# Kernel optimization log

Hardware: AMD Instinct MI355X
Metric: run time of the kernel (lower is better)

Reference implementation:

```python
import jax, jax.numpy as jnp
import numpy as np

B, T, D, H = 2, 2048, 1024, 16
DH = D // H  # 64, rope dim


def rotate_half(x):
    x1, x2 = jnp.split(x, 2, axis=-1)
    return jnp.concatenate([-x2, x1], axis=-1)


def rope_tables(seq_len, dim, dtype=jnp.float32):
    inv_freq = 1.0 / (10000.0 ** (jnp.arange(0, dim, 2, dtype=jnp.float32) / dim))
    t = jnp.arange(seq_len, dtype=jnp.float32)
    freqs = jnp.outer(t, inv_freq)              # [T, dim/2]
    emb = jnp.concatenate([freqs, freqs], -1)   # [T, dim]
    return jnp.cos(emb).astype(dtype), jnp.sin(emb).astype(dtype)


def setup_inputs() -> dict:
    key = jax.random.key(0)
    ks = jax.random.split(key, 5)
    w_scale = 0.02
    x = jax.random.normal(ks[0], (B, T, D), jnp.float32)
    W_q = jax.random.normal(ks[1], (D, D), jnp.float32) * w_scale
    W_k = jax.random.normal(ks[2], (D, D), jnp.float32) * w_scale
    W_v = jax.random.normal(ks[3], (D, D), jnp.float32) * w_scale
    W_o = jax.random.normal(ks[4], (D, D), jnp.float32) * w_scale
    mask = jnp.tril(jnp.ones((T, T), jnp.int32))  # causal
    return {"x": x, "W_q": W_q, "W_k": W_k, "W_v": W_v, "W_o": W_o, "mask": mask}


def reference(x, W_q, W_k, W_v, W_o, mask):
    b, t, d = x.shape
    # Linear (bias=False): y = x @ W^T, weight shape (out, in)
    def proj(W):
        y = jnp.einsum('btd,ed->bte', x, W)
        return y.reshape(b, t, H, DH).transpose(0, 2, 1, 3)  # [B,H,T,dh]
    q, k, v = proj(W_q), proj(W_k), proj(W_v)

    cos, sin = rope_tables(t, DH, x.dtype)
    cos = cos[None, None]  # [1,1,T,dh]
    sin = sin[None, None]
    q = q * cos + rotate_half(q) * sin
    k = k * cos + rotate_half(k) * sin

    scale = 1.0 / np.sqrt(DH).astype(np.float32)
    scores = jnp.einsum('bhqd,bhkd->bhqk', q, k) * scale  # [B,H,T,T]
    neg_inf = jnp.finfo(scores.dtype).min
    scores = jnp.where(mask[:t, :t][None, None] == 0, neg_inf, scores)
    attn = jax.nn.softmax(scores, axis=-1)
    out = jnp.einsum('bhqk,bhkd->bhqd', attn, v)
    out = out.transpose(0, 2, 1, 3).reshape(b, t, d)
    return jnp.einsum('btd,ed->bte', out, W_o)
```

## Files before the change

kernel.cpp:

```cpp
#include <hip/hip_runtime.h>
#include <hip/hip_bf16.h>
#include <math.h>

#define B_  2
#define T_  2048
#define D_  1024
#define H_  16
#define DH_ 64
#define WN_ (D_ * D_)

typedef __attribute__((ext_vector_type(8))) short bf16x8;
typedef __attribute__((ext_vector_type(4))) float f32x4;
typedef __attribute__((ext_vector_type(16))) float f32x16;

__device__ __forceinline__ void gll16(const void* g, void* l) {
  __builtin_amdgcn_global_load_lds(
      (const __attribute__((address_space(1))) void*)g,
      (__attribute__((address_space(3))) void*)l, 16, 0, 0);
}

__device__ __forceinline__ void storeC(float* p, float v) { *p = v; }
__device__ __forceinline__ void storeC(__hip_bfloat16* p, float v) {
  *p = __float2bfloat16(v);
}

__global__ __launch_bounds__(256)
void cvt_f32_bf16(const float* __restrict__ in, __hip_bfloat16* __restrict__ out,
                  int n4) {
  const int i = blockIdx.x * 256 + threadIdx.x;
  if (i >= n4) return;
  const float4 a = ((const float4*)in)[i];
  __hip_bfloat16 h0 = __float2bfloat16(a.x);
  __hip_bfloat16 h1 = __float2bfloat16(a.y);
  __hip_bfloat16 h2 = __float2bfloat16(a.z);
  __hip_bfloat16 h3 = __float2bfloat16(a.w);
  ushort4 o;
  o.x = *(unsigned short*)&h0;
  o.y = *(unsigned short*)&h1;
  o.z = *(unsigned short*)&h2;
  o.w = *(unsigned short*)&h3;
  *(ushort4*)(out + (size_t)i * 4) = o;
}

__global__ __launch_bounds__(256)
void cvt3_w(const float* __restrict__ Wq, const float* __restrict__ Wk,
            const float* __restrict__ Wv, __hip_bfloat16* __restrict__ out) {
  const int i = blockIdx.x * 256 + threadIdx.x;
  const int per = WN_ / 4;
  const int sel = i >> 18;
  const int off = i & (per - 1);
  const float* src = sel == 0 ? Wq : (sel == 1 ? Wk : Wv);
  const float4 a = ((const float4*)src)[off];
  __hip_bfloat16 h0 = __float2bfloat16(a.x);
  __hip_bfloat16 h1 = __float2bfloat16(a.y);
  __hip_bfloat16 h2 = __float2bfloat16(a.z);
  __hip_bfloat16 h3 = __float2bfloat16(a.w);
  ushort4 o;
  o.x = *(unsigned short*)&h0;
  o.y = *(unsigned short*)&h1;
  o.z = *(unsigned short*)&h2;
  o.w = *(unsigned short*)&h3;
  *(ushort4*)(out + (size_t)sel * WN_ + (size_t)off * 4) = o;
}

template <typename CT>
__global__ __launch_bounds__(256)
void gemm_bf16_mfma(const __hip_bfloat16* __restrict__ A,
                    const __hip_bfloat16* __restrict__ W,
                    CT* __restrict__ C, int M, int N, int K) {
  __shared__ unsigned short As[128 * 32];
  __shared__ unsigned short Bs[128 * 32];
  const int tid = threadIdx.x;
  const int w = tid >> 6;
  const int lane = tid & 63;
  const int lg = lane >> 4;
  const int ln = lane & 15;
  const int wr = w >> 1, wc = w & 1;
  const int row0 = blockIdx.y * 128;
  const int col0 = blockIdx.x * 128;

  const int sr = w * 32 + (lane >> 2);
  const int sp = lane & 3;

  f32x4 acc[4][4];
#pragma unroll
  for (int m = 0; m < 4; ++m)
#pragma unroll
    for (int n = 0; n < 4; ++n) acc[m][n] = (f32x4){0.f, 0.f, 0.f, 0.f};

  for (int k0 = 0; k0 < K; k0 += 32) {
#pragma unroll
    for (int c = 0; c < 2; ++c) {
      const int r = sr + c * 16;
      const int ks = sp ^ ((r >> 1) & 3);
      gll16(A + (size_t)(row0 + r) * K + k0 + ks * 8,
            &As[(w * 32 + c * 16) * 32]);
      gll16(W + (size_t)(col0 + r) * K + k0 + ks * 8,
            &Bs[(w * 32 + c * 16) * 32]);
    }
    __syncthreads();

    bf16x8 af[4], bfr[4];
#pragma unroll
    for (int m = 0; m < 4; ++m) {
      const int r = wr * 64 + m * 16 + ln;
      af[m] = *(const bf16x8*)&As[r * 32 + (lg ^ ((r >> 1) & 3)) * 8];
    }
#pragma unroll
    for (int n = 0; n < 4; ++n) {
      const int r = wc * 64 + n * 16 + ln;
      bfr[n] = *(const bf16x8*)&Bs[r * 32 + (lg ^ ((r >> 1) & 3)) * 8];
    }
#pragma unroll
    for (int m = 0; m < 4; ++m)
#pragma unroll
      for (int n = 0; n < 4; ++n)
        acc[m][n] = __builtin_amdgcn_mfma_f32_16x16x32_bf16(af[m], bfr[n],
                                                            acc[m][n], 0, 0, 0);
    __syncthreads();
  }

#pragma unroll
  for (int m = 0; m < 4; ++m) {
#pragma unroll
    for (int reg = 0; reg < 4; ++reg) {
      CT* crow = C + (size_t)(row0 + wr * 64 + m * 16 + lg * 4 + reg) * N
                 + col0 + wc * 64;
#pragma unroll
      for (int n = 0; n < 4; ++n) storeC(&crow[n * 16 + ln], acc[m][n][reg]);
    }
  }
}

__global__ __launch_bounds__(256)
void rope_qkv(const __hip_bfloat16* __restrict__ qkv,
              __hip_bfloat16* __restrict__ Qb, __hip_bfloat16* __restrict__ Kb) {
  const int idx = blockIdx.x * 256 + threadIdx.x;
  const int i = idx & 31;
  const int rest = idx >> 5;
  const int row = rest >> 4;
  const int h = rest & 15;
  const int t = row & (T_ - 1);
  const float inv_freq = powf(10000.0f, -(float)i * (1.0f / 32.0f));
  const float ang = (float)t * inv_freq;
  const float c = cosf(ang), s = sinf(ang);
  const size_t rb = (size_t)row * 3072 + h * 64;
  const float q1 = __bfloat162float(qkv[rb + i]);
  const float q2 = __bfloat162float(qkv[rb + i + 32]);
  const float k1 = __bfloat162float(qkv[rb + 1024 + i]);
  const float k2 = __bfloat162float(qkv[rb + 1024 + i + 32]);
  const size_t base = (size_t)rest * DH_;
  Qb[base + i]      = __float2bfloat16((q1 * c - q2 * s) * 0.125f);
  Qb[base + i + 32] = __float2bfloat16((q2 * c + q1 * s) * 0.125f);
  Kb[base + i]      = __float2bfloat16(k1 * c - k2 * s);
  Kb[base + i + 32] = __float2bfloat16(k2 * c + k1 * s);
}

__global__ __launch_bounds__(256)
void kf_prep(const __hip_bfloat16* __restrict__ kb, __hip_bfloat16* __restrict__ Kf) {
  const int kt = blockIdx.x;
  const int bh = blockIdx.y;
  const int b = bh >> 4, h = bh & 15;
  const int tid = threadIdx.x;
  const int j = tid & 7;
  const int t0 = tid >> 3;
  __hip_bfloat16* dsth = Kf + (size_t)bh * (T_ * 64) + (size_t)kt * 4096;
#pragma unroll
  for (int it = 0; it < 2; ++it) {
    const int t = it * 32 + t0;
    bf16x8 x = *(const bf16x8*)(kb +
        (size_t)(((size_t)b * T_ + kt * 64 + t) * H_ + h) * 64 + j * 8);
    const int kb2 = t >> 5, lane31 = t & 31, ks = j >> 1, hi = j & 1;
    *(bf16x8*)(dsth + (((kb2 * 4 + ks) * 64 + hi * 32 + lane31) * 8)) = x;
  }
}

__global__ __launch_bounds__(256)
void vf_prep(const __hip_bfloat16* __restrict__ qkv, __hip_bfloat16* __restrict__ Vf) {
  __shared__ unsigned short Ls[64][72];
  const int kt = blockIdx.x;
  const int bh = blockIdx.y;
  const int b = bh >> 4, h = bh & 15;
  const int tid = threadIdx.x;
  const int rb = tid >> 3, c0 = (tid & 7) * 8;
#pragma unroll
  for (int it = 0; it < 2; ++it) {
    const int r = it * 32 + rb;
    uint4 x = *(const uint4*)&qkv[(size_t)((size_t)b * T_ + kt * 64 + r) * 3072 +
                                  2048 + h * 64 + c0];
    const unsigned short* xs = (const unsigned short*)&x;
#pragma unroll
    for (int q = 0; q < 8; ++q) Ls[c0 + q][r] = xs[q];
  }
  __syncthreads();
  __hip_bfloat16* dsth = Vf + (size_t)bh * (T_ * 64) + (size_t)kt * 4096;
#pragma unroll
  for (int e = 0; e < 2; ++e) {
    const int g = e * 256 + tid;
    const int lane31 = g & 31, hi = (g >> 5) & 1, ks = (g >> 6) & 3, kb2 = g >> 8;
    bf16x8 x = *(const bf16x8*)&Ls[kb2 * 32 + lane31][ks * 16 + hi * 8];
    *(bf16x8*)(dsth + (size_t)g * 8) = x;
  }
}

#define SWZ(row, col) ((col) ^ (((row) & 7) << 3))

struct KV { bf16x8 k[2][4]; bf16x8 v[2][4]; };

__global__ __launch_bounds__(256, 2)
void attn_reg(const __hip_bfloat16* __restrict__ Qb,
              const __hip_bfloat16* __restrict__ Kf,
              const __hip_bfloat16* __restrict__ Vf,
              __hip_bfloat16* __restrict__ O) {
  __shared__ unsigned short Ps[4][32 * 64];

  const int bx = blockIdx.x;
  const int bh = blockIdx.y;
  const int b = bh >> 4, h = bh & 15;
  const int tid = threadIdx.x;
  const int w = tid >> 6;
  const int lane = tid & 63;
  const int lq = lane & 31;
  const int hi = lane >> 5;

  const int qu = (w < 2) ? (2 * bx + w) : (62 - 2 * bx + (w & 1));
  const int nt = (qu >> 1) + 1;
  const int q_glob = qu * 32 + lq;

  const size_t headoff = (size_t)b * T_ * D_ + (size_t)h * DH_;
  const __hip_bfloat16* Qg = Qb + headoff;
  const __hip_bfloat16* Kfh = Kf + (size_t)bh * (T_ * 64);
  const __hip_bfloat16* Vfh = Vf + (size_t)bh * (T_ * 64);
  __hip_bfloat16* Og = O + headoff;

  bf16x8 qf[4];
#pragma unroll
  for (int ks = 0; ks < 4; ++ks)
    qf[ks] = *(const bf16x8*)(Qg + (size_t)q_glob * D_ + ks * 16 + hi * 8);

  float m_run = -3.0e38f, l_run = 0.f;
  f32x16 accO[2];
#pragma unroll
  for (int reg = 0; reg < 16; ++reg) { accO[0][reg] = 0.f; accO[1][reg] = 0.f; }

  auto load = [&](int kt) {
    KV r;
    const __hip_bfloat16* kp = Kfh + (size_t)kt * 4096;
    const __hip_bfloat16* vp = Vfh + (size_t)kt * 4096;
#pragma unroll
    for (int kb2 = 0; kb2 < 2; ++kb2)
#pragma unroll
      for (int ks = 0; ks < 4; ++ks) {
        r.k[kb2][ks] = *(const bf16x8*)(kp + ((kb2 * 4 + ks) * 64 + lane) * 8);
        r.v[kb2][ks] = *(const bf16x8*)(vp + ((kb2 * 4 + ks) * 64 + lane) * 8);
      }
    return r;
  };

  auto compute = [&](const KV& kv, int kt) {
    f32x16 sf[2];
#pragma unroll
    for (int reg = 0; reg < 16; ++reg) { sf[0][reg] = 0.f; sf[1][reg] = 0.f; }
    const bool last = (kt == nt - 1);
    const bool skip1 = last && !(qu & 1);
#pragma unroll
    for (int ks = 0; ks < 4; ++ks)
      sf[0] = __builtin_amdgcn_mfma_f32_32x32x16_bf16(kv.k[0][ks], qf[ks], sf[0], 0, 0, 0);
    if (!skip1) {
#pragma unroll
      for (int ks = 0; ks < 4; ++ks)
        sf[1] = __builtin_amdgcn_mfma_f32_32x32x16_bf16(kv.k[1][ks], qf[ks], sf[1], 0, 0, 0);
    }

    if (last) {
      const int kv0 = kt * 64;
#pragma unroll
      for (int reg = 0; reg < 16; ++reg) {
        const int krow = (reg & 3) + 8 * (reg >> 2) + 4 * hi;
        if (kv0 + krow > q_glob)      sf[0][reg] = -3.0e38f;
        if (kv0 + 32 + krow > q_glob) sf[1][reg] = -3.0e38f;
      }
    }

    float pmax = -3.0e38f;
#pragma unroll
    for (int reg = 0; reg < 16; ++reg)
      pmax = fmaxf(pmax, fmaxf(sf[0][reg], sf[1][reg]));
    pmax = fmaxf(pmax, __shfl_xor(pmax, 32, 64));
    const float mnew = fmaxf(m_run, pmax);
    const float alpha = __expf(m_run - mnew);
    m_run = mnew;
    float rsum = 0.f;
#pragma unroll
    for (int reg = 0; reg < 16; ++reg) {
      sf[0][reg] = __expf(sf[0][reg] - mnew);
      sf[1][reg] = __expf(sf[1][reg] - mnew);
      rsum += sf[0][reg] + sf[1][reg];
    }
    rsum += __shfl_xor(rsum, 32, 64);
    l_run = l_run * alpha + rsum;
#pragma unroll
    for (int reg = 0; reg < 16; ++reg) {
      accO[0][reg] *= alpha;
      accO[1][reg] *= alpha;
    }

#pragma unroll
    for (int kb2 = 0; kb2 < 2; ++kb2) {
#pragma unroll
      for (int j = 0; j < 4; ++j) {
        __hip_bfloat16 b0 = __float2bfloat16(sf[kb2][4 * j + 0]);
        __hip_bfloat16 b1 = __float2bfloat16(sf[kb2][4 * j + 1]);
        __hip_bfloat16 b2 = __float2bfloat16(sf[kb2][4 * j + 2]);
        __hip_bfloat16 b3 = __float2bfloat16(sf[kb2][4 * j + 3]);
        uint2 pk;
        pk.x = (unsigned)*(unsigned short*)&b0 |
               ((unsigned)*(unsigned short*)&b1 << 16);
        pk.y = (unsigned)*(unsigned short*)&b2 |
               ((unsigned)*(unsigned short*)&b3 << 16);
        const int col = kb2 * 32 + 8 * j + 4 * hi;
        *(uint2*)&Ps[w][lq * 64 + SWZ(lq, col)] = pk;
      }
    }

#pragma unroll
    for (int ks = 0; ks < 4; ++ks) {
      const int c = ks * 16 + hi * 8;
      bf16x8 pb = *(const bf16x8*)&Ps[w][lq * 64 + SWZ(lq, c)];
      accO[0] = __builtin_amdgcn_mfma_f32_32x32x16_bf16(kv.v[0][ks], pb, accO[0], 0, 0, 0);
      accO[1] = __builtin_amdgcn_mfma_f32_32x32x16_bf16(kv.v[1][ks], pb, accO[1], 0, 0, 0);
    }
  };

  KV bufA = load(0), bufB;
  int kt = 0;
  while (true) {
    if (kt + 1 < nt) bufB = load(kt + 1);
    compute(bufA, kt);
    ++kt; if (kt == nt) break;
    if (kt + 1 < nt) bufA = load(kt + 1);
    compute(bufB, kt);
    ++kt; if (kt == nt) break;
  }

  const float inv = 1.0f / l_run;
#pragma unroll
  for (int db = 0; db < 2; ++db) {
#pragma unroll
    for (int j = 0; j < 4; ++j) {
      __hip_bfloat16 b0 = __float2bfloat16(accO[db][4 * j + 0] * inv);
      __hip_bfloat16 b1 = __float2bfloat16(accO[db][4 * j + 1] * inv);
      __hip_bfloat16 b2 = __float2bfloat16(accO[db][4 * j + 2] * inv);
      __hip_bfloat16 b3 = __float2bfloat16(accO[db][4 * j + 3] * inv);
      uint2 pk;
      pk.x = (unsigned)*(unsigned short*)&b0 |
             ((unsigned)*(unsigned short*)&b1 << 16);
      pk.y = (unsigned)*(unsigned short*)&b2 |
             ((unsigned)*(unsigned short*)&b3 << 16);
      const int d = db * 32 + 8 * j + 4 * hi;
      *(uint2*)(Og + (size_t)q_glob * D_ + d) = pk;
    }
  }
}

extern "C" void kernel_launch(void* const* d_in, const int* in_sizes, int n_in,
                              void* d_out, int out_size, void* d_ws, size_t ws_size,
                              hipStream_t stream) {
  const float* x  = (const float*)d_in[0];
  const float* Wq = (const float*)d_in[1];
  const float* Wk = (const float*)d_in[2];
  const float* Wv = (const float*)d_in[3];
  const float* Wo = (const float*)d_in[4];
  float* out = (float*)d_out;

  const size_t NE = (size_t)B_ * T_ * D_;
  char* base = (char*)d_ws;
  __hip_bfloat16* qkvb  = (__hip_bfloat16*)base;
  __hip_bfloat16* xb    = (__hip_bfloat16*)(base + 3 * NE * 2);
  __hip_bfloat16* Wqkvb = (__hip_bfloat16*)(base + 4 * NE * 2);
  __hip_bfloat16* qb    = (__hip_bfloat16*)(base + 4 * NE * 2 + 3ull * WN_ * 2);
  __hip_bfloat16* kb    = qb + NE;
  __hip_bfloat16* Kfb   = kb + NE;
  __hip_bfloat16* Vfb   = Kfb + NE;
  __hip_bfloat16* aob   = qkvb;
  __hip_bfloat16* Wob   = Wqkvb;

  cvt_f32_bf16<<<(int)(NE / 4 / 256), 256, 0, stream>>>(x, xb, (int)(NE / 4));
  cvt3_w<<<3 * WN_ / 4 / 256, 256, 0, stream>>>(Wq, Wk, Wv, Wqkvb);

  const dim3 gq(3 * D_ / 128, (B_ * T_) / 128);
  gemm_bf16_mfma<__hip_bfloat16><<<gq, 256, 0, stream>>>(
      xb, Wqkvb, qkvb, B_ * T_, 3 * D_, D_);

  rope_qkv<<<(B_ * T_ * H_ * 32) / 256, 256, 0, stream>>>(qkvb, qb, kb);
  kf_prep<<<dim3(T_ / 64, B_ * H_), 256, 0, stream>>>(kb, Kfb);
  vf_prep<<<dim3(T_ / 64, B_ * H_), 256, 0, stream>>>(qkvb, Vfb);

  const dim3 ga(16, B_ * H_);
  attn_reg<<<ga, 256, 0, stream>>>(qb, Kfb, Vfb, aob);

  cvt_f32_bf16<<<WN_ / 4 / 256, 256, 0, stream>>>(Wo, Wob, WN_ / 4);

  const dim3 go(D_ / 128, (B_ * T_) / 128);
  gemm_bf16_mfma<float><<<go, 256, 0, stream>>>(aob, Wob, out, B_ * T_, D_, D_);
}
```

Baseline: 234.0 us.

## Split attention KV range across wave pairs and fuse RoPE with K layout prep

The attention kernel now gives each block two query tiles and splits each tile's causal KV range between two waves. The partial accumulators, max and sum are merged through shared memory, and the launch doubles to 1024 blocks with a swizzled block order and occupancy hint 3. RoPE now uses vectorized 8-wide loads and writes K directly in the MFMA-friendly layout, which removes the separate kf_prep kernel and its intermediate buffer. This is meant to raise parallelism and balance the causal work, at the cost of extra LDS for the merge and a block-wide sync.

```diff
diff --git a/kernel.cpp b/kernel.cpp
--- a/kernel.cpp
+++ b/kernel.cpp
@@ -24,21 +24,27 @@
   *p = __float2bfloat16(v);
 }
 
+__device__ __forceinline__ float bf2f(short u) {
+  union { unsigned int i; float f; } cv;
+  cv.i = ((unsigned int)(unsigned short)u) << 16;
+  return cv.f;
+}
+__device__ __forceinline__ short f2bf(float f) {
+  __hip_bfloat16 h = __float2bfloat16(f);
+  return *(short*)&h;
+}
+
 __global__ __launch_bounds__(256)
 void cvt_f32_bf16(const float* __restrict__ in, __hip_bfloat16* __restrict__ out,
                   int n4) {
   const int i = blockIdx.x * 256 + threadIdx.x;
   if (i >= n4) return;
   const float4 a = ((const float4*)in)[i];
-  __hip_bfloat16 h0 = __float2bfloat16(a.x);
-  __hip_bfloat16 h1 = __float2bfloat16(a.y);
-  __hip_bfloat16 h2 = __float2bfloat16(a.z);
-  __hip_bfloat16 h3 = __float2bfloat16(a.w);
   ushort4 o;
-  o.x = *(unsigned short*)&h0;
-  o.y = *(unsigned short*)&h1;
-  o.z = *(unsigned short*)&h2;
-  o.w = *(unsigned short*)&h3;
+  o.x = (unsigned short)f2bf(a.x);
+  o.y = (unsigned short)f2bf(a.y);
+  o.z = (unsigned short)f2bf(a.z);
+  o.w = (unsigned short)f2bf(a.w);
   *(ushort4*)(out + (size_t)i * 4) = o;
 }
 
@@ -51,15 +57,11 @@
   const int off = i & (per - 1);
   const float* src = sel == 0 ? Wq : (sel == 1 ? Wk : Wv);
   const float4 a = ((const float4*)src)[off];
-  __hip_bfloat16 h0 = __float2bfloat16(a.x);
-  __hip_bfloat16 h1 = __float2bfloat16(a.y);
-  __hip_bfloat16 h2 = __float2bfloat16(a.z);
-  __hip_bfloat16 h3 = __float2bfloat16(a.w);
   ushort4 o;
-  o.x = *(unsigned short*)&h0;
-  o.y = *(unsigned short*)&h1;
-  o.z = *(unsigned short*)&h2;
-  o.w = *(unsigned short*)&h3;
+  o.x = (unsigned short)f2bf(a.x);
+  o.y = (unsigned short)f2bf(a.y);
+  o.z = (unsigned short)f2bf(a.z);
+  o.w = (unsigned short)f2bf(a.w);
   *(ushort4*)(out + (size_t)sel * WN_ + (size_t)off * 4) = o;
 }
 
@@ -133,46 +135,45 @@
 }
 
 __global__ __launch_bounds__(256)
-void rope_qkv(const __hip_bfloat16* __restrict__ qkv,
-              __hip_bfloat16* __restrict__ Qb, __hip_bfloat16* __restrict__ Kb) {
+void rope_fused(const __hip_bfloat16* __restrict__ qkv,
+                __hip_bfloat16* __restrict__ Qb,
+                __hip_bfloat16* __restrict__ Kf) {
   const int idx = blockIdx.x * 256 + threadIdx.x;
-  const int i = idx & 31;
-  const int rest = idx >> 5;
+  const int j = idx & 3;
+  const int rest = idx >> 2;
+  const int h = rest & 15;
   const int row = rest >> 4;
-  const int h = rest & 15;
   const int t = row & (T_ - 1);
-  const float inv_freq = powf(10000.0f, -(float)i * (1.0f / 32.0f));
-  const float ang = (float)t * inv_freq;
-  const float c = cosf(ang), s = sinf(ang);
-  const size_t rb = (size_t)row * 3072 + h * 64;
-  const float q1 = __bfloat162float(qkv[rb + i]);
-  const float q2 = __bfloat162float(qkv[rb + i + 32]);
-  const float k1 = __bfloat162float(qkv[rb + 1024 + i]);
-  const float k2 = __bfloat162float(qkv[rb + 1024 + i + 32]);
-  const size_t base = (size_t)rest * DH_;
-  Qb[base + i]      = __float2bfloat16((q1 * c - q2 * s) * 0.125f);
-  Qb[base + i + 32] = __float2bfloat16((q2 * c + q1 * s) * 0.125f);
-  Kb[base + i]      = __float2bfloat16(k1 * c - k2 * s);
-  Kb[base + i + 32] = __float2bfloat16(k2 * c + k1 * s);
-}
-
-__global__ __launch_bounds__(256)
-void kf_prep(const __hip_bfloat16* __restrict__ kb, __hip_bfloat16* __restrict__ Kf) {
-  const int kt = blockIdx.x;
-  const int bh = blockIdx.y;
-  const int b = bh >> 4, h = bh & 15;
-  const int tid = threadIdx.x;
-  const int j = tid & 7;
-  const int t0 = tid >> 3;
-  __hip_bfloat16* dsth = Kf + (size_t)bh * (T_ * 64) + (size_t)kt * 4096;
-#pragma unroll
-  for (int it = 0; it < 2; ++it) {
-    const int t = it * 32 + t0;
-    bf16x8 x = *(const bf16x8*)(kb +
-        (size_t)(((size_t)b * T_ + kt * 64 + t) * H_ + h) * 64 + j * 8);
-    const int kb2 = t >> 5, lane31 = t & 31, ks = j >> 1, hi = j & 1;
-    *(bf16x8*)(dsth + (((kb2 * 4 + ks) * 64 + hi * 32 + lane31) * 8)) = x;
-  }
+  const int b = row >> 11;
+
+  const size_t src = (size_t)row * 3072 + h * 64 + j * 8;
+  bf16x8 qlo = *(const bf16x8*)(qkv + src);
+  bf16x8 qhi = *(const bf16x8*)(qkv + src + 32);
+  bf16x8 klo = *(const bf16x8*)(qkv + src + 1024);
+  bf16x8 khi = *(const bf16x8*)(qkv + src + 1024 + 32);
+  bf16x8 qolo, qohi, kolo, kohi;
+#pragma unroll
+  for (int i = 0; i < 8; ++i) {
+    const int d = j * 8 + i;
+    const float inv_freq = powf(10000.0f, -(float)d * (1.0f / 32.0f));
+    const float ang = (float)t * inv_freq;
+    const float c = cosf(ang), s = sinf(ang);
+    const float q1 = bf2f(qlo[i]), q2 = bf2f(qhi[i]);
+    const float k1 = bf2f(klo[i]), k2 = bf2f(khi[i]);
+    qolo[i] = f2bf((q1 * c - q2 * s) * 0.125f);
+    qohi[i] = f2bf((q2 * c + q1 * s) * 0.125f);
+    kolo[i] = f2bf(k1 * c - k2 * s);
+    kohi[i] = f2bf(k2 * c + k1 * s);
+  }
+  __hip_bfloat16* qdst = Qb + (size_t)rest * 64 + j * 8;
+  *(bf16x8*)qdst = qolo;
+  *(bf16x8*)(qdst + 32) = qohi;
+
+  const int bh = b * 16 + h, kt = t >> 6, tt = t & 63;
+  const int kb2 = tt >> 5, l31 = tt & 31, ks = j >> 1, hb = j & 1;
+  __hip_bfloat16* kdst = Kf + (size_t)bh * (T_ * 64) + (size_t)kt * 4096;
+  *(bf16x8*)(kdst + ((kb2 * 4 + ks) * 64 + hb * 32 + l31) * 8) = kolo;
+  *(bf16x8*)(kdst + ((kb2 * 4 + ks + 2) * 64 + hb * 32 + l31) * 8) = kohi;
 }
 
 __global__ __launch_bounds__(256)
@@ -207,26 +208,36 @@
 
 struct KV { bf16x8 k[2][4]; bf16x8 v[2][4]; };
 
-__global__ __launch_bounds__(256, 2)
-void attn_reg(const __hip_bfloat16* __restrict__ Qb,
-              const __hip_bfloat16* __restrict__ Kf,
-              const __hip_bfloat16* __restrict__ Vf,
-              __hip_bfloat16* __restrict__ O) {
+__global__ __launch_bounds__(256, 3)
+void attn_split(const __hip_bfloat16* __restrict__ Qb,
+                const __hip_bfloat16* __restrict__ Kf,
+                const __hip_bfloat16* __restrict__ Vf,
+                __hip_bfloat16* __restrict__ O) {
   __shared__ unsigned short Ps[4][32 * 64];
-
-  const int bx = blockIdx.x;
-  const int bh = blockIdx.y;
-  const int b = bh >> 4, h = bh & 15;
+  __shared__ float MrgAcc[2][64][33];
+  __shared__ float MrgML[2][64][2];
+
+  const int id = (int)blockIdx.x + 32 * (int)blockIdx.y;
+  const int nid = (id & 7) * 128 + (id >> 3);
+  const int bx = nid & 31;
+  const int bh = nid >> 5;
+
   const int tid = threadIdx.x;
   const int w = tid >> 6;
   const int lane = tid & 63;
   const int lq = lane & 31;
   const int hi = lane >> 5;
-
-  const int qu = (w < 2) ? (2 * bx + w) : (62 - 2 * bx + (w & 1));
+  const int slot = w >> 1;
+  const int half = w & 1;
+
+  const int qu = slot ? (63 - bx) : bx;
   const int nt = (qu >> 1) + 1;
+  const int nA = nt - (nt >> 1);
+  const int kt0 = half ? nA : 0;
+  const int kt1 = half ? nt : nA;
   const int q_glob = qu * 32 + lq;
 
+  const int b = bh >> 4, h = bh & 15;
   const size_t headoff = (size_t)b * T_ * D_ + (size_t)h * DH_;
   const __hip_bfloat16* Qg = Qb + headoff;
   const __hip_bfloat16* Kfh = Kf + (size_t)bh * (T_ * 64);
@@ -309,15 +320,11 @@
     for (int kb2 = 0; kb2 < 2; ++kb2) {
 #pragma unroll
       for (int j = 0; j < 4; ++j) {
-        __hip_bfloat16 b0 = __float2bfloat16(sf[kb2][4 * j + 0]);
-        __hip_bfloat16 b1 = __float2bfloat16(sf[kb2][4 * j + 1]);
-        __hip_bfloat16 b2 = __float2bfloat16(sf[kb2][4 * j + 2]);
-        __hip_bfloat16 b3 = __float2bfloat16(sf[kb2][4 * j + 3]);
         uint2 pk;
-        pk.x = (unsigned)*(unsigned short*)&b0 |
-               ((unsigned)*(unsigned short*)&b1 << 16);
-        pk.y = (unsigned)*(unsigned short*)&b2 |
-               ((unsigned)*(unsigned short*)&b3 << 16);
+        pk.x = (unsigned)(unsigned short)f2bf(sf[kb2][4 * j + 0]) |
+               ((unsigned)(unsigned short)f2bf(sf[kb2][4 * j + 1]) << 16);
+        pk.y = (unsigned)(unsigned short)f2bf(sf[kb2][4 * j + 2]) |
+               ((unsigned)(unsigned short)f2bf(sf[kb2][4 * j + 3]) << 16);
         const int col = kb2 * 32 + 8 * j + 4 * hi;
         *(uint2*)&Ps[w][lq * 64 + SWZ(lq, col)] = pk;
       }
@@ -332,33 +339,52 @@
     }
   };
 
-  KV bufA = load(0), bufB;
-  int kt = 0;
-  while (true) {
-    if (kt + 1 < nt) bufB = load(kt + 1);
-    compute(bufA, kt);
-    ++kt; if (kt == nt) break;
-    if (kt + 1 < nt) bufA = load(kt + 1);
-    compute(bufB, kt);
-    ++kt; if (kt == nt) break;
-  }
-
-  const float inv = 1.0f / l_run;
-#pragma unroll
-  for (int db = 0; db < 2; ++db) {
-#pragma unroll
-    for (int j = 0; j < 4; ++j) {
-      __hip_bfloat16 b0 = __float2bfloat16(accO[db][4 * j + 0] * inv);
-      __hip_bfloat16 b1 = __float2bfloat16(accO[db][4 * j + 1] * inv);
-      __hip_bfloat16 b2 = __float2bfloat16(accO[db][4 * j + 2] * inv);
-      __hip_bfloat16 b3 = __float2bfloat16(accO[db][4 * j + 3] * inv);
-      uint2 pk;
-      pk.x = (unsigned)*(unsigned short*)&b0 |
-             ((unsigned)*(unsigned short*)&b1 << 16);
-      pk.y = (unsigned)*(unsigned short*)&b2 |
-             ((unsigned)*(unsigned short*)&b3 << 16);
-      const int d = db * 32 + 8 * j + 4 * hi;
-      *(uint2*)(Og + (size_t)q_glob * D_ + d) = pk;
+  if (kt0 < kt1) {
+    KV bufA = load(kt0), bufB;
+    int kt = kt0;
+    while (true) {
+      if (kt + 1 < kt1) bufB = load(kt + 1);
+      compute(bufA, kt);
+      ++kt; if (kt == kt1) break;
+      if (kt + 1 < kt1) bufA = load(kt + 1);
+      compute(bufB, kt);
+      ++kt; if (kt == kt1) break;
+    }
+  }
+
+  if (half) {
+#pragma unroll
+    for (int reg = 0; reg < 16; ++reg) {
+      MrgAcc[slot][lane][reg] = accO[0][reg];
+      MrgAcc[slot][lane][16 + reg] = accO[1][reg];
+    }
+    MrgML[slot][lane][0] = m_run;
+    MrgML[slot][lane][1] = l_run;
+  }
+  __syncthreads();
+  if (!half) {
+    const float mB = MrgML[slot][lane][0];
+    const float lB = MrgML[slot][lane][1];
+    const float mS = fmaxf(m_run, mB);
+    const float aA = __expf(m_run - mS);
+    const float aB = __expf(mB - mS);
+    const float linv = 1.0f / (l_run * aA + lB * aB);
+#pragma unroll
+    for (int db = 0; db < 2; ++db) {
+#pragma unroll
+      for (int j = 0; j < 4; ++j) {
+        float o0 = (accO[db][4 * j + 0] * aA + MrgAcc[slot][lane][db * 16 + 4 * j + 0] * aB) * linv;
+        float o1 = (accO[db][4 * j + 1] * aA + MrgAcc[slot][lane][db * 16 + 4 * j + 1] * aB) * linv;
+        float o2 = (accO[db][4 * j + 2] * aA + MrgAcc[slot][lane][db * 16 + 4 * j + 2] * aB) * linv;
+        float o3 = (accO[db][4 * j + 3] * aA + MrgAcc[slot][lane][db * 16 + 4 * j + 3] * aB) * linv;
+        uint2 pk;
+        pk.x = (unsigned)(unsigned short)f2bf(o0) |
+               ((unsigned)(unsigned short)f2bf(o1) << 16);
+        pk.y = (unsigned)(unsigned short)f2bf(o2) |
+               ((unsigned)(unsigned short)f2bf(o3) << 16);
+        const int d = db * 32 + 8 * j + 4 * hi;
+        *(uint2*)(Og + (size_t)q_glob * D_ + d) = pk;
+      }
     }
   }
 }
@@ -379,8 +405,7 @@
   __hip_bfloat16* xb    = (__hip_bfloat16*)(base + 3 * NE * 2);
   __hip_bfloat16* Wqkvb = (__hip_bfloat16*)(base + 4 * NE * 2);
   __hip_bfloat16* qb    = (__hip_bfloat16*)(base + 4 * NE * 2 + 3ull * WN_ * 2);
-  __hip_bfloat16* kb    = qb + NE;
-  __hip_bfloat16* Kfb   = kb + NE;
+  __hip_bfloat16* Kfb   = qb + NE;
   __hip_bfloat16* Vfb   = Kfb + NE;
   __hip_bfloat16* aob   = qkvb;
   __hip_bfloat16* Wob   = Wqkvb;
@@ -392,12 +417,11 @@
   gemm_bf16_mfma<__hip_bfloat16><<<gq, 256, 0, stream>>>(
       xb, Wqkvb, qkvb, B_ * T_, 3 * D_, D_);
 
-  rope_qkv<<<(B_ * T_ * H_ * 32) / 256, 256, 0, stream>>>(qkvb, qb, kb);
-  kf_prep<<<dim3(T_ / 64, B_ * H_), 256, 0, stream>>>(kb, Kfb);
+  rope_fused<<<(B_ * T_ * H_ * 4) / 256, 256, 0, stream>>>(qkvb, qb, Kfb);
   vf_prep<<<dim3(T_ / 64, B_ * H_), 256, 0, stream>>>(qkvb, Vfb);
 
-  const dim3 ga(16, B_ * H_);
-  attn_reg<<<ga, 256, 0, stream>>>(qb, Kfb, Vfb, aob);
+  const dim3 ga(32, 32);
+  attn_split<<<ga, 256, 0, stream>>>(qb, Kfb, Vfb, aob);
 
   cvt_f32_bf16<<<WN_ / 4 / 256, 256, 0, stream>>>(Wo, Wob, WN_ / 4);
 
```

Result: slower. 379.8 us (+62.3%).
